# Kernel optimization log

Hardware: AMD Instinct MI355X
Metric: run time of the kernel (lower is better)

## Reference

```python
import jax, jax.numpy as jnp
import numpy as np

NS, NG, E = 4096, 20000, 131072   # samples, genes, edges per relation
DIN, H, C1, C3 = 256, 4, 64, 128  # input dim, heads, layer1 per-head, layer3 per-head


def _gatv2(xs, xd, src, dst, Wl, bl, Wr, br, att, bias, num_dst, out_c, concat):
    """PyG GATv2Conv (add_self_loops=False, no edge_attr), eval mode."""
    xl = (xs @ Wl + bl).reshape(-1, H, out_c)  # [Nsrc,H,C] transformed sources
    xr = (xd @ Wr + br).reshape(-1, H, out_c)  # [Ndst,H,C] transformed targets
    g = jax.nn.leaky_relu(xl[src] + xr[dst], 0.2)          # [E,H,C]
    alpha = jnp.einsum('ehc,hc->eh', g, att)               # [E,H]
    m = jax.ops.segment_max(alpha, dst, num_segments=num_dst)
    ea = jnp.exp(alpha - m[dst])
    den = jax.ops.segment_sum(ea, dst, num_segments=num_dst)
    a = ea / (den[dst] + 1e-16)                            # segment softmax over in-edges
    out = jax.ops.segment_sum(a[:, :, None] * xl[src], dst, num_segments=num_dst)  # [Ndst,H,C]
    out = out.reshape(num_dst, H * out_c) if concat else out.mean(axis=1)
    return out + bias


def setup_inputs() -> dict:
    key = jax.random.key(0)
    ks = jax.random.split(key, 24)
    w = lambda k, s: jax.random.normal(k, s, jnp.float32) * 0.05
    d = {}
    d['x_sample'] = jax.random.normal(ks[0], (NS, DIN), jnp.float32)
    d['x_gene'] = jax.random.normal(ks[1], (NG, DIN), jnp.float32)
    d['sg_src'] = jax.random.randint(ks[2], (E,), 0, NS)
    d['sg_dst'] = jax.random.randint(ks[3], (E,), 0, NG)
    d['gs_src'] = jax.random.randint(ks[4], (E,), 0, NG)
    d['gs_dst'] = jax.random.randint(ks[5], (E,), 0, NS)
    i = 6
    for rel in ('sg', 'gs'):
        d[f'Wl1_{rel}'] = w(ks[i], (DIN, H * C1)); i += 1
        d[f'bl1_{rel}'] = jnp.zeros((H * C1,), jnp.float32)
        d[f'Wr1_{rel}'] = w(ks[i], (DIN, H * C1)); i += 1
        d[f'br1_{rel}'] = jnp.zeros((H * C1,), jnp.float32)
        d[f'att1_{rel}'] = w(ks[i], (H, C1)); i += 1
        d[f'bias1_{rel}'] = jnp.zeros((H * C1,), jnp.float32)
    d['Wl3_gs'] = w(ks[i], (H * C1, H * C3)); i += 1
    d['bl3_gs'] = jnp.zeros((H * C3,), jnp.float32)
    d['Wr3_gs'] = w(ks[i], (H * C1, H * C3)); i += 1
    d['br3_gs'] = jnp.zeros((H * C3,), jnp.float32)
    d['att3_gs'] = w(ks[i], (H, C3)); i += 1
    d['bias3_gs'] = jnp.zeros((C3,), jnp.float32)
    d['sl1_W'] = w(ks[i], (DIN, C1)); i += 1
    d['sl1_b'] = jnp.zeros((C1,), jnp.float32)
    d['sl3_W'] = w(ks[i], (H * C1, C3)); i += 1
    d['sl3_b'] = jnp.zeros((C3,), jnp.float32)
    return d


def reference(x_sample, x_gene, sg_src, sg_dst, gs_src, gs_dst,
              Wl1_sg, bl1_sg, Wr1_sg, br1_sg, att1_sg, bias1_sg,
              Wl1_gs, bl1_gs, Wr1_gs, br1_gs, att1_gs, bias1_gs,
              Wl3_gs, bl3_gs, Wr3_gs, br3_gs, att3_gs, bias3_gs,
              sl1_W, sl1_b, sl3_W, sl3_b):
    # layer 1 (HeteroConv: one GATv2 per relation, concat heads)
    x1_gene = _gatv2(x_sample, x_gene, sg_src, sg_dst,
                     Wl1_sg, bl1_sg, Wr1_sg, br1_sg, att1_sg, bias1_sg, NG, C1, True)
    x1_sample = _gatv2(x_gene, x_sample, gs_src, gs_dst,
                       Wl1_gs, bl1_gs, Wr1_gs, br1_gs, att1_gs, bias1_gs, NS, C1, True)
    # self-loop linear (only for omic/sample nodes), repeated across heads
    x1_sample = x1_sample + jnp.tile(x_sample @ sl1_W + sl1_b, (1, H))
    x1_sample = jax.nn.elu(x1_sample)
    x1_gene = jax.nn.elu(x1_gene)
    # three_layers=False -> x2 = x1; layer 3 (concat=False -> head mean)
    x3_sample = _gatv2(x1_gene, x1_sample, gs_src, gs_dst,
                       Wl3_gs, bl3_gs, Wr3_gs, br3_gs, att3_gs, bias3_gs, NS, C3, False)
    x3_sample = x3_sample + (x1_sample @ sl3_W + sl3_b)
    x3_sample = jax.nn.elu(x3_sample)
    # stack over 1 omic channel -> transpose -> integrator=None -> squeeze
    return x3_sample  # [NS, C3]
```

## Files before the change

### kernel.cpp

```cpp
#include <hip/hip_runtime.h>
#include <hip/hip_bf16.h>
#include <cstdint>

constexpr int kNS = 4096;
constexpr int kNG = 20000;
constexpr int kE  = 131072;
constexpr int kNCAT = kNG + kNS;
constexpr int kNB = (kNCAT + 255) / 256;
constexpr float kL2E = 1.4426950408889634f;

typedef __attribute__((ext_vector_type(8))) short short8;
typedef __attribute__((ext_vector_type(4))) float f32x4;
typedef __attribute__((ext_vector_type(2))) float f32x2;

__device__ __forceinline__ float elu_f(float v) { return v > 0.f ? v : expm1f(v); }

__device__ __forceinline__ unsigned short f2bf(float f) {
  union { float f; unsigned u; } v; v.f = f;
  unsigned r = v.u + 0x7FFF + ((v.u >> 16) & 1);
  return (unsigned short)(r >> 16);
}

__device__ __forceinline__ float bf2f(unsigned short u) {
  union { unsigned u; float f; } v; v.u = ((unsigned)u) << 16; return v.f;
}

__device__ __forceinline__ f32x2 bfp2(unsigned u) {
  union { unsigned u; float f; } lo, hi;
  lo.u = u << 16; hi.u = u & 0xffff0000u;
  return (f32x2){lo.f, hi.f};
}

__global__ __launch_bounds__(256) void zero_int(int* __restrict__ p, int n) {
  int i = blockIdx.x * 256 + threadIdx.x;
  if (i < n) p[i] = 0;
}

__global__ __launch_bounds__(256) void prep(
    const float* __restrict__ xs, const float* __restrict__ xg,
    const float* __restrict__ Wl1_sg, const float* __restrict__ Wr1_gs,
    const float* __restrict__ sl1_W, const float* __restrict__ Wr1_sg,
    const float* __restrict__ Wl1_gs, const float* __restrict__ Wl3,
    const float* __restrict__ Wr3, const float* __restrict__ sl3_W,
    const float* __restrict__ bl1_sg, const float* __restrict__ br1_gs,
    const float* __restrict__ sl1_b, const float* __restrict__ br1_sg,
    const float* __restrict__ bl1_gs, const float* __restrict__ br3,
    const float* __restrict__ sl3_b,
    const int* __restrict__ sg_dst, const int* __restrict__ gs_dst,
    int* __restrict__ deg_g, int* __restrict__ deg_s,
    unsigned short* __restrict__ xs_bf, unsigned short* __restrict__ xg_bf,
    unsigned short* __restrict__ Wt1, unsigned short* __restrict__ Wt2,
    unsigned short* __restrict__ Wt3, unsigned short* __restrict__ Wt4,
    float* __restrict__ bc1, float* __restrict__ bc2, float* __restrict__ bc4) {
  int bid = blockIdx.x, tid = threadIdx.x;
  if (bid < 1024) {
    int i = (bid * 256 + tid) * 4;
    float4 v = *(const float4*)&xs[i];
    ushort4 o = {f2bf(v.x), f2bf(v.y), f2bf(v.z), f2bf(v.w)};
    *(ushort4*)&xs_bf[i] = o;
    return;
  }
  bid -= 1024;
  if (bid < 5000) {
    int i = (bid * 256 + tid) * 4;
    float4 v = *(const float4*)&xg[i];
    ushort4 o = {f2bf(v.x), f2bf(v.y), f2bf(v.z), f2bf(v.w)};
    *(ushort4*)&xg_bf[i] = o;
    return;
  }
  bid -= 5000;
  auto wseg = [&](const float* W, unsigned short* Wt, int N) {
    int i = bid * 256 + tid;
    int n = i >> 8, k = i & 255;
    Wt[i] = f2bf(W[(size_t)k * N + n]);
  };
  if (bid < 256) { wseg(Wl1_sg, Wt1, 256); return; } bid -= 256;
  if (bid < 256) { wseg(Wr1_gs, Wt1 + 256 * 256, 256); return; } bid -= 256;
  if (bid < 64)  { wseg(sl1_W,  Wt1 + 512 * 256, 64);  return; } bid -= 64;
  if (bid < 256) { wseg(Wr1_sg, Wt2, 256); return; } bid -= 256;
  if (bid < 256) { wseg(Wl1_gs, Wt2 + 256 * 256, 256); return; } bid -= 256;
  if (bid < 512) { wseg(Wl3,    Wt3, 512); return; } bid -= 512;
  if (bid < 512) { wseg(Wr3,    Wt4, 512); return; } bid -= 512;
  if (bid < 128) { wseg(sl3_W,  Wt4 + 512 * 256, 128); return; } bid -= 128;
  if (bid < 7) {
    int j = bid * 256 + tid;
    if (j < 256) bc1[j] = bl1_sg[j];
    else if (j < 512) bc1[j] = br1_gs[j - 256];
    else if (j < 576) bc1[j] = sl1_b[j - 512];
    else if (j < 832) bc2[j - 576] = br1_sg[j - 576];
    else if (j < 1088) bc2[j - 576] = bl1_gs[j - 832];
    else if (j < 1600) bc4[j - 1088] = br3[j - 1088];
    else if (j < 1728) bc4[j - 1088] = sl3_b[j - 1600];
    return;
  }
  bid -= 7;
  int i = bid * 256 + tid;
  if (i < kE) atomicAdd(&deg_g[sg_dst[i]], 1);
  else atomicAdd(&deg_s[gs_dst[i - kE]], 1);
}

__global__ __launch_bounds__(256) void scan_fused(
    int* __restrict__ deg, int* __restrict__ rp_g, int* __restrict__ rp_s,
    int* __restrict__ pval, int* __restrict__ pflag) {
  int b = blockIdx.x, t = threadIdx.x;
  int i = b * 256 + t;
  int v = i < kNCAT ? deg[i] : 0;
  __shared__ int s[256];
  s[t] = v;
  __syncthreads();
  for (int ofs = 1; ofs < 256; ofs <<= 1) {
    int add = t >= ofs ? s[t - ofs] : 0;
    __syncthreads();
    s[t] += add;
    __syncthreads();
  }
  if (t == 255) {
    atomicExch(&pval[b], s[255]);
    __threadfence();
    atomicExch(&pflag[b], 1);
  }
  int pre = 0;
  if (t < b) {
    while (atomicAdd(&pflag[t], 0) == 0) {}
    pre = atomicAdd(&pval[t], 0);
  }
  pre += __shfl_xor(pre, 1);  pre += __shfl_xor(pre, 2);
  pre += __shfl_xor(pre, 4);  pre += __shfl_xor(pre, 8);
  pre += __shfl_xor(pre, 16); pre += __shfl_xor(pre, 32);
  __shared__ int ws4[4];
  if ((t & 63) == 0) ws4[t >> 6] = pre;
  __syncthreads();
  int prefix = ws4[0] + ws4[1] + ws4[2] + ws4[3];
  int ex = prefix + s[t] - v;
  if (i < kNG) { rp_g[i] = ex; deg[i] = 0; }
  else if (i < kNCAT) { rp_s[i - kNG] = ex - kE; deg[i] = 0; }
  if (b == 0 && t == 0) { rp_g[kNG] = kE; rp_s[kNS] = kE; }
}

__device__ __forceinline__ void gemm_body(
    const unsigned short* __restrict__ A, const unsigned short* __restrict__ Bt,
    const float* __restrict__ bias, unsigned short* __restrict__ Cb,
    int M, int N, int bx, int by) {
  __shared__ alignas(16) unsigned short As[128 * 32];
  __shared__ alignas(16) unsigned short Bs[64 * 32];
  const int tid = threadIdx.x;
  const int wave = tid >> 6, lane = tid & 63;
  const int brow = by * 128, bcol = bx * 64;
  const int wrow = (wave >> 1) * 64, wcol = (wave & 1) * 32;
  const int la = lane & 15, lk = (lane >> 4) * 8;
  f32x4 acc[4][2] = {};
  for (int k0 = 0; k0 < 256; k0 += 32) {
#pragma unroll
    for (int c = 0; c < 2; ++c) {
      int seg = wave * 128 + c * 64 + lane;
      int row = seg >> 2, ks = (seg & 3) * 8;
      int grow = brow + row; if (grow > M - 1) grow = M - 1;
      const unsigned short* g = A + (size_t)grow * 256 + k0 + ks;
      __builtin_amdgcn_global_load_lds(
          (const __attribute__((address_space(1))) unsigned*)g,
          (__attribute__((address_space(3))) unsigned*)&As[(wave * 128 + c * 64) * 8],
          16, 0, 0);
    }
    {
      int seg = wave * 64 + lane;
      int row = seg >> 2, ks = (seg & 3) * 8;
      const unsigned short* g = Bt + (size_t)(bcol + row) * 256 + k0 + ks;
      __builtin_amdgcn_global_load_lds(
          (const __attribute__((address_space(1))) unsigned*)g,
          (__attribute__((address_space(3))) unsigned*)&Bs[(wave * 64) * 8],
          16, 0, 0);
    }
    __syncthreads();
    short8 bfr[2];
#pragma unroll
    for (int ni = 0; ni < 2; ++ni)
      bfr[ni] = *(const short8*)&Bs[(wcol + ni * 16 + la) * 32 + lk];
#pragma unroll
    for (int mi = 0; mi < 4; ++mi) {
      short8 af = *(const short8*)&As[(wrow + mi * 16 + la) * 32 + lk];
#pragma unroll
      for (int ni = 0; ni < 2; ++ni)
        acc[mi][ni] = __builtin_amdgcn_mfma_f32_16x16x32_bf16(af, bfr[ni], acc[mi][ni], 0, 0, 0);
    }
    __syncthreads();
  }
  const int r0 = (lane >> 4) * 4;
#pragma unroll
  for (int mi = 0; mi < 4; ++mi) {
#pragma unroll
    for (int r = 0; r < 4; ++r) {
      int row = brow + wrow + mi * 16 + r0 + r;
      if (row >= M) continue;
#pragma unroll
      for (int ni = 0; ni < 2; ++ni) {
        int col = bcol + wcol + ni * 16 + la;
        Cb[(size_t)row * N + col] = f2bf(acc[mi][ni][r] + bias[col]);
      }
    }
  }
}

__global__ __launch_bounds__(256) void gemm_build(
    const unsigned short* __restrict__ A0, const unsigned short* __restrict__ B0,
    const float* __restrict__ b0, unsigned short* __restrict__ C0, int M0, int N0, int nb0,
    const unsigned short* __restrict__ A1, const unsigned short* __restrict__ B1,
    const float* __restrict__ b1, unsigned short* __restrict__ C1, int M1, int N1, int nb1,
    const int* __restrict__ sgd, const int* __restrict__ sgs,
    const int* __restrict__ rpg, int* __restrict__ curg, int* __restrict__ psg,
    const int* __restrict__ gsd, const int* __restrict__ gss,
    const int* __restrict__ rps, int* __restrict__ curs, int* __restrict__ pss) {
  int flat = blockIdx.x;
  if (flat < nb0) {
    int nbx = N0 / 64;
    gemm_body(A0, B0, b0, C0, M0, N0, flat % nbx, flat / nbx);
    return;
  }
  flat -= nb0;
  if (flat < nb1) {
    int nbx = N1 / 64;
    gemm_body(A1, B1, b1, C1, M1, N1, flat % nbx, flat / nbx);
    return;
  }
  flat -= nb1;
  int i = flat * 256 + threadIdx.x;
  if (i < kE) {
    int d = sgd[i];
    psg[rpg[d] + atomicAdd(&curg[d], 1)] = sgs[i];
  } else {
    i -= kE;
    int d = gsd[i];
    pss[rps[d] + atomicAdd(&curs[d], 1)] = gss[i];
  }
}

template <bool SPLIT, bool ADDSL>
__device__ __forceinline__ void gat64_body(
    const unsigned short* __restrict__ xl, int ldl,
    const unsigned short* __restrict__ xr, int ldr,
    const float* __restrict__ att,
    const int* __restrict__ psrc, const int* __restrict__ rp,
    const float* __restrict__ bias,
    const unsigned short* __restrict__ sl, int ldsl,
    unsigned short* __restrict__ out, int N, int rbid) {
  int tid = threadIdx.x;
  int cl = tid & 31;
  int d, sub;
  if (SPLIT) { d = rbid * 4 + (tid >> 6); sub = (tid >> 5) & 1; }
  else       { d = rbid * 8 + (tid >> 5); sub = 0; }
  if (d >= N) return;
  f32x2 xr2[4], at2[4];
  {
    const uint4 xu = *(const uint4*)&xr[(size_t)d * ldr + cl * 8];
    xr2[0] = bfp2(xu.x); xr2[1] = bfp2(xu.y); xr2[2] = bfp2(xu.z); xr2[3] = bfp2(xu.w);
    float4 a0 = *(const float4*)&att[cl * 8];
    float4 a1 = *(const float4*)&att[cl * 8 + 4];
    at2[0] = (f32x2){a0.x, a0.y} * kL2E; at2[1] = (f32x2){a0.z, a0.w} * kL2E;
    at2[2] = (f32x2){a1.x, a1.y} * kL2E; at2[3] = (f32x2){a1.z, a1.w} * kL2E;
  }
  float l = 0.f;
  f32x2 acc2[4] = {};
  int i0 = rp[d], i1 = rp[d + 1];
  for (int i = SPLIT ? i0 + sub * 4 : i0; i < i1; i += SPLIT ? 8 : 4) {
    int ia = i + 1 < i1 ? i + 1 : i;
    int ib = i + 2 < i1 ? i + 2 : i;
    int ic = i + 3 < i1 ? i + 3 : i;
    int s0 = psrc[i], s1 = psrc[ia], s2 = psrc[ib], s3 = psrc[ic];
    uint4 xu0 = *(const uint4*)&xl[(size_t)s0 * ldl + cl * 8];
    uint4 xu1 = *(const uint4*)&xl[(size_t)s1 * ldl + cl * 8];
    uint4 xu2 = *(const uint4*)&xl[(size_t)s2 * ldl + cl * 8];
    uint4 xu3 = *(const uint4*)&xl[(size_t)s3 * ldl + cl * 8];
    f32x2 xf[4][4];
    xf[0][0] = bfp2(xu0.x); xf[0][1] = bfp2(xu0.y); xf[0][2] = bfp2(xu0.z); xf[0][3] = bfp2(xu0.w);
    xf[1][0] = bfp2(xu1.x); xf[1][1] = bfp2(xu1.y); xf[1][2] = bfp2(xu1.z); xf[1][3] = bfp2(xu1.w);
    xf[2][0] = bfp2(xu2.x); xf[2][1] = bfp2(xu2.y); xf[2][2] = bfp2(xu2.z); xf[2][3] = bfp2(xu2.w);
    xf[3][0] = bfp2(xu3.x); xf[3][1] = bfp2(xu3.y); xf[3][2] = bfp2(xu3.z); xf[3][3] = bfp2(xu3.w);
    float dt[4];
#pragma unroll
    for (int b = 0; b < 4; ++b) {
      f32x2 d2 = {0.f, 0.f};
#pragma unroll
      for (int p = 0; p < 4; ++p) {
        f32x2 v = xf[b][p] + xr2[p];
        f32x2 lk = __builtin_elementwise_max(v, v * 0.2f);
        d2 = __builtin_elementwise_fma(lk, at2[p], d2);
      }
      float dd = d2.x + d2.y;
      dd += __shfl_xor(dd, 1);
      dd += __shfl_xor(dd, 2);
      dd += __shfl_xor(dd, 4);
      dt[b] = dd;
    }
    float w0 = exp2f(dt[0]);
    float w1 = (i + 1 < i1) ? exp2f(dt[1]) : 0.f;
    float w2 = (i + 2 < i1) ? exp2f(dt[2]) : 0.f;
    float w3 = (i + 3 < i1) ? exp2f(dt[3]) : 0.f;
    l += (w0 + w1) + (w2 + w3);
#pragma unroll
    for (int p = 0; p < 4; ++p) {
      acc2[p] = __builtin_elementwise_fma(xf[0][p], (f32x2){w0, w0}, acc2[p]);
      acc2[p] = __builtin_elementwise_fma(xf[1][p], (f32x2){w1, w1}, acc2[p]);
      acc2[p] = __builtin_elementwise_fma(xf[2][p], (f32x2){w2, w2}, acc2[p]);
      acc2[p] = __builtin_elementwise_fma(xf[3][p], (f32x2){w3, w3}, acc2[p]);
    }
  }
  if (SPLIT) {
    l += __shfl_xor(l, 32);
#pragma unroll
    for (int p = 0; p < 4; ++p) {
      acc2[p].x += __shfl_xor(acc2[p].x, 32);
      acc2[p].y += __shfl_xor(acc2[p].y, 32);
    }
    if (sub != 0) return;
  }
  float dinv = 1.f / (l + 1e-16f);
  short8 o;
#pragma unroll
  for (int p = 0; p < 4; ++p) {
    int c = cl * 8 + p * 2;
    float v0 = acc2[p].x * dinv + bias[c];
    float v1 = acc2[p].y * dinv + bias[c + 1];
    if (ADDSL) {
      v0 += bf2f(sl[(size_t)d * ldsl + (c & 63)]);
      v1 += bf2f(sl[(size_t)d * ldsl + ((c + 1) & 63)]);
    }
    o[p * 2]     = (short)f2bf(elu_f(v0));
    o[p * 2 + 1] = (short)f2bf(elu_f(v1));
  }
  *(short8*)&out[(size_t)d * 256 + cl * 8] = o;
}

__global__ __launch_bounds__(256) void gat12(
    const unsigned short* __restrict__ xlA, int ldlA,
    const unsigned short* __restrict__ xrA, int ldrA,
    const float* __restrict__ attA, const int* __restrict__ psA,
    const int* __restrict__ rpA, const float* __restrict__ biasA,
    unsigned short* __restrict__ outA, int NA, int nbA,
    const unsigned short* __restrict__ xlB, int ldlB,
    const unsigned short* __restrict__ xrB, int ldrB,
    const float* __restrict__ attB, const int* __restrict__ psB,
    const int* __restrict__ rpB, const float* __restrict__ biasB,
    const unsigned short* __restrict__ slB, int ldslB,
    unsigned short* __restrict__ outB, int NB) {
  int bid = blockIdx.x;
  if (bid < nbA)
    gat64_body<false, false>(xlA, ldlA, xrA, ldrA, attA, psA, rpA, biasA,
                             nullptr, 0, outA, NA, bid);
  else
    gat64_body<true, true>(xlB, ldlB, xrB, ldrB, attB, psB, rpB, biasB,
                           slB, ldslB, outB, NB, bid - nbA);
}

__global__ __launch_bounds__(256) void gat3(
    const unsigned short* __restrict__ xl,
    const unsigned short* __restrict__ xr,
    const float* __restrict__ att,
    const int* __restrict__ psrc, const int* __restrict__ rp,
    const float* __restrict__ bias,
    const unsigned short* __restrict__ sl,
    float* __restrict__ out) {
  __shared__ float sm_acc[2][64][8];
  __shared__ float sm_l[2][64];
  int w = threadIdx.x >> 6, lane = threadIdx.x & 63;
  int p = w >> 1, wp = w & 1;
  int d = blockIdx.x * 2 + p;
  f32x2 xr2[4], at2[4];
  {
    const uint4 xu = *(const uint4*)&xr[(size_t)d * 640 + lane * 8];
    xr2[0] = bfp2(xu.x); xr2[1] = bfp2(xu.y); xr2[2] = bfp2(xu.z); xr2[3] = bfp2(xu.w);
    float4 a0 = *(const float4*)&att[lane * 8];
    float4 a1 = *(const float4*)&att[lane * 8 + 4];
    at2[0] = (f32x2){a0.x, a0.y} * kL2E; at2[1] = (f32x2){a0.z, a0.w} * kL2E;
    at2[2] = (f32x2){a1.x, a1.y} * kL2E; at2[3] = (f32x2){a1.z, a1.w} * kL2E;
  }
  float l = 0.f;
  f32x2 acc2[4] = {};
  int i0 = rp[d], i1 = rp[d + 1];
  for (int i = i0 + wp * 4; i < i1; i += 8) {
    int ia = i + 1 < i1 ? i + 1 : i;
    int ib = i + 2 < i1 ? i + 2 : i;
    int ic = i + 3 < i1 ? i + 3 : i;
    int s0 = psrc[i], s1 = psrc[ia], s2 = psrc[ib], s3 = psrc[ic];
    uint4 xu0 = *(const uint4*)&xl[(size_t)s0 * 512 + lane * 8];
    uint4 xu1 = *(const uint4*)&xl[(size_t)s1 * 512 + lane * 8];
    uint4 xu2 = *(const uint4*)&xl[(size_t)s2 * 512 + lane * 8];
    uint4 xu3 = *(const uint4*)&xl[(size_t)s3 * 512 + lane * 8];
    f32x2 xf[4][4];
    xf[0][0] = bfp2(xu0.x); xf[0][1] = bfp2(xu0.y); xf[0][2] = bfp2(xu0.z); xf[0][3] = bfp2(xu0.w);
    xf[1][0] = bfp2(xu1.x); xf[1][1] = bfp2(xu1.y); xf[1][2] = bfp2(xu1.z); xf[1][3] = bfp2(xu1.w);
    xf[2][0] = bfp2(xu2.x); xf[2][1] = bfp2(xu2.y); xf[2][2] = bfp2(xu2.z); xf[2][3] = bfp2(xu2.w);
    xf[3][0] = bfp2(xu3.x); xf[3][1] = bfp2(xu3.y); xf[3][2] = bfp2(xu3.z); xf[3][3] = bfp2(xu3.w);
    float dt[4];
#pragma unroll
    for (int b = 0; b < 4; ++b) {
      f32x2 d2 = {0.f, 0.f};
#pragma unroll
      for (int q = 0; q < 4; ++q) {
        f32x2 v = xf[b][q] + xr2[q];
        f32x2 lk = __builtin_elementwise_max(v, v * 0.2f);
        d2 = __builtin_elementwise_fma(lk, at2[q], d2);
      }
      float dd = d2.x + d2.y;
      dd += __shfl_xor(dd, 1);
      dd += __shfl_xor(dd, 2);
      dd += __shfl_xor(dd, 4);
      dd += __shfl_xor(dd, 8);
      dt[b] = dd;
    }
    float w0 = exp2f(dt[0]);
    float w1 = (i + 1 < i1) ? exp2f(dt[1]) : 0.f;
    float w2 = (i + 2 < i1) ? exp2f(dt[2]) : 0.f;
    float w3 = (i + 3 < i1) ? exp2f(dt[3]) : 0.f;
    l += (w0 + w1) + (w2 + w3);
#pragma unroll
    for (int q = 0; q < 4; ++q) {
      acc2[q] = __builtin_elementwise_fma(xf[0][q], (f32x2){w0, w0}, acc2[q]);
      acc2[q] = __builtin_elementwise_fma(xf[1][q], (f32x2){w1, w1}, acc2[q]);
      acc2[q] = __builtin_elementwise_fma(xf[2][q], (f32x2){w2, w2}, acc2[q]);
      acc2[q] = __builtin_elementwise_fma(xf[3][q], (f32x2){w3, w3}, acc2[q]);
    }
  }
  if (wp == 1) {
#pragma unroll
    for (int q = 0; q < 4; ++q) {
      sm_acc[p][lane][q * 2]     = acc2[q].x;
      sm_acc[p][lane][q * 2 + 1] = acc2[q].y;
    }
    sm_l[p][lane] = l;
  }
  __syncthreads();
  if (wp == 0) {
    l += sm_l[p][lane];
    float dinv = 1.f / (l + 1e-16f);
    float r[8];
#pragma unroll
    for (int q = 0; q < 4; ++q) {
      r[q * 2]     = (acc2[q].x + sm_acc[p][lane][q * 2]) * dinv;
      r[q * 2 + 1] = (acc2[q].y + sm_acc[p][lane][q * 2 + 1]) * dinv;
    }
#pragma unroll
    for (int j = 0; j < 8; ++j) {
      r[j] += __shfl_xor(r[j], 16);
      r[j] += __shfl_xor(r[j], 32);
    }
    if (lane < 16) {
#pragma unroll
      for (int j = 0; j < 8; ++j) {
        int c = lane * 8 + j;
        out[(size_t)d * 128 + c] =
            elu_f(0.25f * r[j] + bias[c] + bf2f(sl[(size_t)d * 640 + c]));
      }
    }
  }
}

extern "C" void kernel_launch(void* const* d_in, const int* in_sizes, int n_in,
                              void* d_out, int out_size, void* d_ws, size_t ws_size,
                              hipStream_t stream) {
  const float* x_sample = (const float*)d_in[0];
  const float* x_gene   = (const float*)d_in[1];
  const int* sg_src = (const int*)d_in[2];
  const int* sg_dst = (const int*)d_in[3];
  const int* gs_src = (const int*)d_in[4];
  const int* gs_dst = (const int*)d_in[5];
  const float* Wl1_sg = (const float*)d_in[6];
  const float* bl1_sg = (const float*)d_in[7];
  const float* Wr1_sg = (const float*)d_in[8];
  const float* br1_sg = (const float*)d_in[9];
  const float* att1_sg = (const float*)d_in[10];
  const float* bias1_sg = (const float*)d_in[11];
  const float* Wl1_gs = (const float*)d_in[12];
  const float* bl1_gs = (const float*)d_in[13];
  const float* Wr1_gs = (const float*)d_in[14];
  const float* br1_gs = (const float*)d_in[15];
  const float* att1_gs = (const float*)d_in[16];
  const float* bias1_gs = (const float*)d_in[17];
  const float* Wl3 = (const float*)d_in[18];
  const float* bl3 = (const float*)d_in[19];
  const float* Wr3 = (const float*)d_in[20];
  const float* br3 = (const float*)d_in[21];
  const float* att3 = (const float*)d_in[22];
  const float* bias3 = (const float*)d_in[23];
  const float* sl1_W = (const float*)d_in[24];
  const float* sl1_b = (const float*)d_in[25];
  const float* sl3_W = (const float*)d_in[26];
  const float* sl3_b = (const float*)d_in[27];

  float* ws = (float*)d_ws;
  size_t off = 0;
  auto alloc = [&](size_t n) { float* p = ws + off; off += n; return p; };
  float* bc1 = alloc(576);
  float* bc2 = alloc(512);
  float* bc4 = alloc(640);
  unsigned short* cat1 = (unsigned short*)alloc((size_t)kNS * 576 / 2);
  unsigned short* cat2 = (unsigned short*)alloc((size_t)kNG * 512 / 2);
  unsigned short* xl3  = (unsigned short*)alloc((size_t)kNG * 512 / 2);
  unsigned short* cat4 = (unsigned short*)alloc((size_t)kNS * 640 / 2);
  unsigned short* xs_bf  = (unsigned short*)alloc((size_t)kNS * 256 / 2);
  unsigned short* xg_bf  = (unsigned short*)alloc((size_t)kNG * 256 / 2);
  unsigned short* xg1_bf = (unsigned short*)alloc((size_t)kNG * 256 / 2);
  unsigned short* xs1_bf = (unsigned short*)alloc((size_t)kNS * 256 / 2);
  unsigned short* Wt1 = (unsigned short*)alloc(576 * 256 / 2);
  unsigned short* Wt2 = (unsigned short*)alloc(512 * 256 / 2);
  unsigned short* Wt3 = (unsigned short*)alloc(512 * 256 / 2);
  unsigned short* Wt4 = (unsigned short*)alloc(640 * 256 / 2);
  int* deg_g  = (int*)alloc(kNG);
  int* deg_s  = (int*)alloc(kNS);
  int* pval   = (int*)alloc(128);
  int* pflag  = (int*)alloc(128);
  int* rp_g   = (int*)alloc(kNG + 1);
  int* rp_s   = (int*)alloc(kNS + 1);
  int* psrc_g = (int*)alloc(kE);
  int* psrc_s = (int*)alloc(kE);

  zero_int<<<(kNCAT + 256 + 255) / 256, 256, 0, stream>>>(deg_g, kNCAT + 256);

  prep<<<9295, 256, 0, stream>>>(
      x_sample, x_gene, Wl1_sg, Wr1_gs, sl1_W, Wr1_sg, Wl1_gs, Wl3, Wr3, sl3_W,
      bl1_sg, br1_gs, sl1_b, br1_sg, bl1_gs, br3, sl3_b,
      sg_dst, gs_dst, deg_g, deg_s,
      xs_bf, xg_bf, Wt1, Wt2, Wt3, Wt4, bc1, bc2, bc4);

  scan_fused<<<kNB, 256, 0, stream>>>(deg_g, rp_g, rp_s, pval, pflag);

  gemm_build<<<288 + 1256 + 1024, 256, 0, stream>>>(
      xs_bf, Wt1, bc1, cat1, kNS, 576, 288,
      xg_bf, Wt2, bc2, cat2, kNG, 512, 1256,
      sg_dst, sg_src, rp_g, deg_g, psrc_g,
      gs_dst, gs_src, rp_s, deg_s, psrc_s);

  gat12<<<2500 + 1024, 256, 0, stream>>>(
      cat1, 576, cat2, 512, att1_sg, psrc_g, rp_g, bias1_sg, xg1_bf, kNG, 2500,
      cat2 + 256, 512, cat1 + 256, 576, att1_gs, psrc_s, rp_s, bias1_gs,
      cat1 + 512, 576, xs1_bf, kNS);

  gemm_build<<<1256 + 320, 256, 0, stream>>>(
      xg1_bf, Wt3, bl3, xl3, kNG, 512, 1256,
      xs1_bf, Wt4, bc4, cat4, kNS, 640, 320,
      sg_dst, sg_src, rp_g, deg_g, psrc_g,
      gs_dst, gs_src, rp_s, deg_s, psrc_s);

  gat3<<<kNS / 2, 256, 0, stream>>>(
      xl3, cat4, att3, psrc_s, rp_s, bias3, cat4 + 512, (float*)d_out);
}
```

Measured before the change: 158.2 us.

## Tile weight transposes, prescale CSR source offsets, pad edge lists, use fast intrinsics

The weight transpose in prep now goes through a 64x64 shared-memory tile, so both reads and writes are coalesced, and it uses far fewer blocks. The CSR build stores source indices already multiplied by the row stride. This lets the gather loops in gat12 and gat3 drop the per-edge clamp and multiply; the edge arrays get 8 zeroed padding entries so reads past the segment end stay in bounds. exp2f and the division are replaced with the AMDGCN hardware exp2 and rcp intrinsics, which trades a small amount of accuracy for fewer instructions.

```diff
diff --git a/kernel.cpp b/kernel.cpp
--- a/kernel.cpp
+++ b/kernel.cpp
@@ -31,9 +31,15 @@
   return (f32x2){lo.f, hi.f};
 }
 
-__global__ __launch_bounds__(256) void zero_int(int* __restrict__ p, int n) {
+__global__ __launch_bounds__(256) void zero_int(int* __restrict__ p, int n,
+                                                int* __restrict__ padA,
+                                                int* __restrict__ padB) {
   int i = blockIdx.x * 256 + threadIdx.x;
   if (i < n) p[i] = 0;
+  if (blockIdx.x == 0 && threadIdx.x < 8) {
+    padA[threadIdx.x] = 0;
+    padB[threadIdx.x] = 0;
+  }
 }
 
 __global__ __launch_bounds__(256) void prep(
@@ -52,6 +58,7 @@
     unsigned short* __restrict__ Wt1, unsigned short* __restrict__ Wt2,
     unsigned short* __restrict__ Wt3, unsigned short* __restrict__ Wt4,
     float* __restrict__ bc1, float* __restrict__ bc2, float* __restrict__ bc4) {
+  __shared__ float tile[64][65];
   int bid = blockIdx.x, tid = threadIdx.x;
   if (bid < 1024) {
     int i = (bid * 256 + tid) * 4;
@@ -69,19 +76,90 @@
     return;
   }
   bid -= 5000;
-  auto wseg = [&](const float* W, unsigned short* Wt, int N) {
-    int i = bid * 256 + tid;
-    int n = i >> 8, k = i & 255;
-    Wt[i] = f2bf(W[(size_t)k * N + n]);
+  auto wtile = [&](const float* W, unsigned short* Wt, int N, int b) {
+    int ntn = N >> 6;
+    int tn = b % ntn, tk = b / ntn;
+    int c = tid & 63, rb = tid >> 6;
+#pragma unroll
+    for (int w = 0; w < 16; ++w) {
+      int r = rb + w * 4;
+      tile[r][c] = W[(size_t)(tk * 64 + r) * N + tn * 64 + c];
+    }
+    __syncthreads();
+#pragma unroll
+    for (int w = 0; w < 16; ++w) {
+      int n = rb + w * 4;
+      Wt[(size_t)(tn * 64 + n) * 256 + tk * 64 + c] = f2bf(tile[c][n]);
+    }
   };
-  if (bid < 256) { wseg(Wl1_sg, Wt1, 256); return; } bid -= 256;
-  if (bid < 256) { wseg(Wr1_gs, Wt1 + 256 * 256, 256); return; } bid -= 256;
-  if (bid < 64)  { wseg(sl1_W,  Wt1 + 512 * 256, 64);  return; } bid -= 64;
-  if (bid < 256) { wseg(Wr1_sg, Wt2, 256); return; } bid -= 256;
-  if (bid < 256) { wseg(Wl1_gs, Wt2 + 256 * 256, 256); return; } bid -= 256;
-  if (bid < 512) { wseg(Wl3,    Wt3, 512); return; } bid -= 512;
-  if (bid < 512) { wseg(Wr3,    Wt4, 512); return; } bid -= 512;
-  if (bid < 128) { wseg(sl3_W,  Wt4 + 512 * 256, 128); return; } bid -= 128;
+  if (bid < 36) {
+    if (bid < 4 * 4 + 20) {}
+    int ntn = 9, tn = bid % ntn, tk = bid / ntn;
+    int c = tid & 63, rb = tid >> 6;
+    int ncol = tn * 64;
+#pragma unroll
+    for (int w = 0; w < 16; ++w) {
+      int r = rb + w * 4;
+      int col = ncol + c;
+      float v;
+      if (col < 256) v = Wl1_sg[(size_t)(tk * 64 + r) * 256 + col];
+      else if (col < 512) v = Wr1_gs[(size_t)(tk * 64 + r) * 256 + (col - 256)];
+      else v = sl1_W[(size_t)(tk * 64 + r) * 64 + (col - 512)];
+      tile[r][c] = v;
+    }
+    __syncthreads();
+#pragma unroll
+    for (int w = 0; w < 16; ++w) {
+      int n = rb + w * 4;
+      Wt1[(size_t)(ncol + n) * 256 + tk * 64 + c] = f2bf(tile[c][n]);
+    }
+    return;
+  }
+  bid -= 36;
+  if (bid < 32) {
+    int ntn = 8, tn = bid % ntn, tk = bid / ntn;
+    int c = tid & 63, rb = tid >> 6;
+    int ncol = tn * 64;
+#pragma unroll
+    for (int w = 0; w < 16; ++w) {
+      int r = rb + w * 4;
+      int col = ncol + c;
+      float v = col < 256 ? Wr1_sg[(size_t)(tk * 64 + r) * 256 + col]
+                          : Wl1_gs[(size_t)(tk * 64 + r) * 256 + (col - 256)];
+      tile[r][c] = v;
+    }
+    __syncthreads();
+#pragma unroll
+    for (int w = 0; w < 16; ++w) {
+      int n = rb + w * 4;
+      Wt2[(size_t)(ncol + n) * 256 + tk * 64 + c] = f2bf(tile[c][n]);
+    }
+    return;
+  }
+  bid -= 32;
+  if (bid < 32) { wtile(Wl3, Wt3, 512, bid); return; }
+  bid -= 32;
+  if (bid < 40) {
+    int ntn = 10, tn = bid % ntn, tk = bid / ntn;
+    int c = tid & 63, rb = tid >> 6;
+    int ncol = tn * 64;
+#pragma unroll
+    for (int w = 0; w < 16; ++w) {
+      int r = rb + w * 4;
+      int col = ncol + c;
+      float v = col < 512 ? Wr3[(size_t)(tk * 64 + r) * 512 + col]
+                          : sl3_W[(size_t)(tk * 64 + r) * 128 + (col - 512)];
+      tile[r][c] = v;
+    }
+    __syncthreads();
+#pragma unroll
+    for (int w = 0; w < 16; ++w) {
+      int n = rb + w * 4;
+      Wt4[(size_t)(ncol + n) * 256 + tk * 64 + c] = f2bf(tile[c][n]);
+    }
+    return;
+  }
+  bid -= 40;
   if (bid < 7) {
     int j = bid * 256 + tid;
     if (j < 256) bc1[j] = bl1_sg[j];
@@ -225,17 +303,17 @@
   int i = flat * 256 + threadIdx.x;
   if (i < kE) {
     int d = sgd[i];
-    psg[rpg[d] + atomicAdd(&curg[d], 1)] = sgs[i];
+    psg[rpg[d] + atomicAdd(&curg[d], 1)] = sgs[i] * 576;
   } else {
     i -= kE;
     int d = gsd[i];
-    pss[rps[d] + atomicAdd(&curs[d], 1)] = gss[i];
+    pss[rps[d] + atomicAdd(&curs[d], 1)] = gss[i] * 512;
   }
 }
 
 template <bool SPLIT, bool ADDSL>
 __device__ __forceinline__ void gat64_body(
-    const unsigned short* __restrict__ xl, int ldl,
+    const unsigned short* __restrict__ xl,
     const unsigned short* __restrict__ xr, int ldr,
     const float* __restrict__ att,
     const int* __restrict__ psrc, const int* __restrict__ rp,
@@ -248,6 +326,7 @@
   if (SPLIT) { d = rbid * 4 + (tid >> 6); sub = (tid >> 5) & 1; }
   else       { d = rbid * 8 + (tid >> 5); sub = 0; }
   if (d >= N) return;
+  const unsigned short* xlb = xl + cl * 8;
   f32x2 xr2[4], at2[4];
   {
     const uint4 xu = *(const uint4*)&xr[(size_t)d * ldr + cl * 8];
@@ -261,14 +340,11 @@
   f32x2 acc2[4] = {};
   int i0 = rp[d], i1 = rp[d + 1];
   for (int i = SPLIT ? i0 + sub * 4 : i0; i < i1; i += SPLIT ? 8 : 4) {
-    int ia = i + 1 < i1 ? i + 1 : i;
-    int ib = i + 2 < i1 ? i + 2 : i;
-    int ic = i + 3 < i1 ? i + 3 : i;
-    int s0 = psrc[i], s1 = psrc[ia], s2 = psrc[ib], s3 = psrc[ic];
-    uint4 xu0 = *(const uint4*)&xl[(size_t)s0 * ldl + cl * 8];
-    uint4 xu1 = *(const uint4*)&xl[(size_t)s1 * ldl + cl * 8];
-    uint4 xu2 = *(const uint4*)&xl[(size_t)s2 * ldl + cl * 8];
-    uint4 xu3 = *(const uint4*)&xl[(size_t)s3 * ldl + cl * 8];
+    int o0 = psrc[i], o1 = psrc[i + 1], o2 = psrc[i + 2], o3 = psrc[i + 3];
+    uint4 xu0 = *(const uint4*)&xlb[o0];
+    uint4 xu1 = *(const uint4*)&xlb[o1];
+    uint4 xu2 = *(const uint4*)&xlb[o2];
+    uint4 xu3 = *(const uint4*)&xlb[o3];
     f32x2 xf[4][4];
     xf[0][0] = bfp2(xu0.x); xf[0][1] = bfp2(xu0.y); xf[0][2] = bfp2(xu0.z); xf[0][3] = bfp2(xu0.w);
     xf[1][0] = bfp2(xu1.x); xf[1][1] = bfp2(xu1.y); xf[1][2] = bfp2(xu1.z); xf[1][3] = bfp2(xu1.w);
@@ -290,10 +366,10 @@
       dd += __shfl_xor(dd, 4);
       dt[b] = dd;
     }
-    float w0 = exp2f(dt[0]);
-    float w1 = (i + 1 < i1) ? exp2f(dt[1]) : 0.f;
-    float w2 = (i + 2 < i1) ? exp2f(dt[2]) : 0.f;
-    float w3 = (i + 3 < i1) ? exp2f(dt[3]) : 0.f;
+    float w0 = __builtin_amdgcn_exp2f(dt[0]);
+    float w1 = (i + 1 < i1) ? __builtin_amdgcn_exp2f(dt[1]) : 0.f;
+    float w2 = (i + 2 < i1) ? __builtin_amdgcn_exp2f(dt[2]) : 0.f;
+    float w3 = (i + 3 < i1) ? __builtin_amdgcn_exp2f(dt[3]) : 0.f;
     l += (w0 + w1) + (w2 + w3);
 #pragma unroll
     for (int p = 0; p < 4; ++p) {
@@ -312,7 +388,7 @@
     }
     if (sub != 0) return;
   }
-  float dinv = 1.f / (l + 1e-16f);
+  float dinv = __builtin_amdgcn_rcpf(l + 1e-16f);
   short8 o;
 #pragma unroll
   for (int p = 0; p < 4; ++p) {
@@ -330,12 +406,12 @@
 }
 
 __global__ __launch_bounds__(256) void gat12(
-    const unsigned short* __restrict__ xlA, int ldlA,
+    const unsigned short* __restrict__ xlA,
     const unsigned short* __restrict__ xrA, int ldrA,
     const float* __restrict__ attA, const int* __restrict__ psA,
     const int* __restrict__ rpA, const float* __restrict__ biasA,
     unsigned short* __restrict__ outA, int NA, int nbA,
-    const unsigned short* __restrict__ xlB, int ldlB,
+    const unsigned short* __restrict__ xlB,
     const unsigned short* __restrict__ xrB, int ldrB,
     const float* __restrict__ attB, const int* __restrict__ psB,
     const int* __restrict__ rpB, const float* __restrict__ biasB,
@@ -343,10 +419,10 @@
     unsigned short* __restrict__ outB, int NB) {
   int bid = blockIdx.x;
   if (bid < nbA)
-    gat64_body<false, false>(xlA, ldlA, xrA, ldrA, attA, psA, rpA, biasA,
+    gat64_body<false, false>(xlA, xrA, ldrA, attA, psA, rpA, biasA,
                              nullptr, 0, outA, NA, bid);
   else
-    gat64_body<true, true>(xlB, ldlB, xrB, ldrB, attB, psB, rpB, biasB,
+    gat64_body<true, true>(xlB, xrB, ldrB, attB, psB, rpB, biasB,
                            slB, ldslB, outB, NB, bid - nbA);
 }
 
@@ -363,6 +439,7 @@
   int w = threadIdx.x >> 6, lane = threadIdx.x & 63;
   int p = w >> 1, wp = w & 1;
   int d = blockIdx.x * 2 + p;
+  const unsigned short* xlb = xl + lane * 8;
   f32x2 xr2[4], at2[4];
   {
     const uint4 xu = *(const uint4*)&xr[(size_t)d * 640 + lane * 8];
@@ -376,14 +453,11 @@
   f32x2 acc2[4] = {};
   int i0 = rp[d], i1 = rp[d + 1];
   for (int i = i0 + wp * 4; i < i1; i += 8) {
-    int ia = i + 1 < i1 ? i + 1 : i;
-    int ib = i + 2 < i1 ? i + 2 : i;
-    int ic = i + 3 < i1 ? i + 3 : i;
-    int s0 = psrc[i], s1 = psrc[ia], s2 = psrc[ib], s3 = psrc[ic];
-    uint4 xu0 = *(const uint4*)&xl[(size_t)s0 * 512 + lane * 8];
-    uint4 xu1 = *(const uint4*)&xl[(size_t)s1 * 512 + lane * 8];
-    uint4 xu2 = *(const uint4*)&xl[(size_t)s2 * 512 + lane * 8];
-    uint4 xu3 = *(const uint4*)&xl[(size_t)s3 * 512 + lane * 8];
+    int o0 = psrc[i], o1 = psrc[i + 1], o2 = psrc[i + 2], o3 = psrc[i + 3];
+    uint4 xu0 = *(const uint4*)&xlb[o0];
+    uint4 xu1 = *(const uint4*)&xlb[o1];
+    uint4 xu2 = *(const uint4*)&xlb[o2];
+    uint4 xu3 = *(const uint4*)&xlb[o3];
     f32x2 xf[4][4];
     xf[0][0] = bfp2(xu0.x); xf[0][1] = bfp2(xu0.y); xf[0][2] = bfp2(xu0.z); xf[0][3] = bfp2(xu0.w);
     xf[1][0] = bfp2(xu1.x); xf[1][1] = bfp2(xu1.y); xf[1][2] = bfp2(xu1.z); xf[1][3] = bfp2(xu1.w);
@@ -406,10 +480,10 @@
       dd += __shfl_xor(dd, 8);
       dt[b] = dd;
     }
-    float w0 = exp2f(dt[0]);
-    float w1 = (i + 1 < i1) ? exp2f(dt[1]) : 0.f;
-    float w2 = (i + 2 < i1) ? exp2f(dt[2]) : 0.f;
-    float w3 = (i + 3 < i1) ? exp2f(dt[3]) : 0.f;
+    float w0 = __builtin_amdgcn_exp2f(dt[0]);
+    float w1 = (i + 1 < i1) ? __builtin_amdgcn_exp2f(dt[1]) : 0.f;
+    float w2 = (i + 2 < i1) ? __builtin_amdgcn_exp2f(dt[2]) : 0.f;
+    float w3 = (i + 3 < i1) ? __builtin_amdgcn_exp2f(dt[3]) : 0.f;
     l += (w0 + w1) + (w2 + w3);
 #pragma unroll
     for (int q = 0; q < 4; ++q) {
@@ -430,7 +504,7 @@
   __syncthreads();
   if (wp == 0) {
     l += sm_l[p][lane];
-    float dinv = 1.f / (l + 1e-16f);
+    float dinv = __builtin_amdgcn_rcpf(l + 1e-16f);
     float r[8];
 #pragma unroll
     for (int q = 0; q < 4; ++q) {
@@ -509,12 +583,13 @@
   int* pflag  = (int*)alloc(128);
   int* rp_g   = (int*)alloc(kNG + 1);
   int* rp_s   = (int*)alloc(kNS + 1);
-  int* psrc_g = (int*)alloc(kE);
-  int* psrc_s = (int*)alloc(kE);
-
-  zero_int<<<(kNCAT + 256 + 255) / 256, 256, 0, stream>>>(deg_g, kNCAT + 256);
-
-  prep<<<9295, 256, 0, stream>>>(
+  int* psrc_g = (int*)alloc(kE + 8);
+  int* psrc_s = (int*)alloc(kE + 8);
+
+  zero_int<<<(kNCAT + 256 + 255) / 256, 256, 0, stream>>>(
+      deg_g, kNCAT + 256, psrc_g + kE, psrc_s + kE);
+
+  prep<<<7195, 256, 0, stream>>>(
       x_sample, x_gene, Wl1_sg, Wr1_gs, sl1_W, Wr1_sg, Wl1_gs, Wl3, Wr3, sl3_W,
       bl1_sg, br1_gs, sl1_b, br1_sg, bl1_gs, br3, sl3_b,
       sg_dst, gs_dst, deg_g, deg_s,
@@ -529,8 +604,8 @@
       gs_dst, gs_src, rp_s, deg_s, psrc_s);
 
   gat12<<<2500 + 1024, 256, 0, stream>>>(
-      cat1, 576, cat2, 512, att1_sg, psrc_g, rp_g, bias1_sg, xg1_bf, kNG, 2500,
-      cat2 + 256, 512, cat1 + 256, 576, att1_gs, psrc_s, rp_s, bias1_gs,
+      cat1, cat2, 512, att1_sg, psrc_g, rp_g, bias1_sg, xg1_bf, kNG, 2500,
+      cat2 + 256, cat1 + 256, 576, att1_gs, psrc_s, rp_s, bias1_gs,
       cat1 + 512, 576, xs1_bf, kNS);
 
   gemm_build<<<1256 + 320, 256, 0, stream>>>(
```

Result: slower. 162.2 us (+2.5%).
